# Performance work log

Measured on AMD Instinct MI355X. Metric: run time of the kernel, lower is better.

Reference implementation:

```python
import jax, jax.numpy as jnp
import numpy as np

N = 50000   # total nodes across batch of graphs
E = 600000  # edges (avg degree 12)
D = 128     # feature dim
L = 3       # GNN layers
B = 64      # number of graphs


def setup_inputs() -> dict:
    key = jax.random.key(0)
    ks = jax.random.split(key, 9)
    x = jax.random.normal(ks[0], (N, D), dtype=jnp.float32)
    edge_index = jax.random.randint(ks[1], (2, E), 0, N)
    batch = jnp.sort(jax.random.randint(ks[2], (N,), 0, B))
    # hard one-hot architecture gates (output of ST gumbel-softmax)
    z_agg = jax.nn.one_hot(jax.random.randint(ks[3], (L,), 0, 3), 3, dtype=jnp.float32)
    z_pool = jax.nn.one_hot(jax.random.randint(ks[4], (), 0, 3), 3, dtype=jnp.float32)
    scale = 1.0 / np.sqrt(D)
    W1 = jax.random.normal(ks[5], (L, D, D), dtype=jnp.float32) * scale
    b1 = jnp.zeros((L, D), dtype=jnp.float32)
    W2 = jax.random.normal(ks[6], (L, D, D), dtype=jnp.float32) * scale
    b2 = jnp.zeros((L, D), dtype=jnp.float32)
    return {"x": x, "edge_index": edge_index, "batch": batch,
            "z_agg": z_agg, "z_pool": z_pool,
            "W1": W1, "b1": b1, "W2": W2, "b2": b2}


def reference(x, edge_index, batch, z_agg, z_pool, W1, b1, W2, b2):
    src, dst = edge_index[0], edge_index[1]
    ones_e = jnp.ones((E,), dtype=x.dtype)
    deg = jax.ops.segment_sum(ones_e, dst, num_segments=N)          # [N]
    deg_c = jnp.maximum(deg, 1.0)[:, None]
    has_nb = (deg > 0)[:, None]

    for l in range(L):
        msg = x[src]                                                # [E, D] gather
        s = jax.ops.segment_sum(msg, dst, num_segments=N)           # sum aggr
        m = s / deg_c                                               # mean aggr
        mx = jax.ops.segment_max(msg, dst, num_segments=N)          # max aggr
        mx = jnp.where(has_nb, mx, 0.0)                             # PyG fills empty with 0
        agg = z_agg[l, 0] * s + z_agg[l, 1] * m + z_agg[l, 2] * mx
        # combine='sum' then FeedForwardNetwork: Linear->relu->Linear
        h = x + agg
        h = jnp.maximum(h @ W1[l] + b1[l], 0.0)
        h = h @ W2[l] + b2[l]
        # act='relu', layer_connect='skip_sum'
        x = x + jnp.maximum(h, 0.0)

    # global pooling mixture over batch vector
    ps = jax.ops.segment_sum(x, batch, num_segments=B)              # [B, D]
    cnt = jax.ops.segment_sum(jnp.ones((N,), x.dtype), batch, num_segments=B)
    pm = ps / jnp.maximum(cnt, 1.0)[:, None]
    pmx = jax.ops.segment_max(x, batch, num_segments=B)
    pmx = jnp.where((cnt > 0)[:, None], pmx, 0.0)
    return z_pool[0] * ps + z_pool[1] * pm + z_pool[2] * pmx
```

## Files before the change

kernel.cpp:

```cpp
#include <hip/hip_runtime.h>
#include <cfloat>

#define DD 128
#define NLAYERS 3
#define NPB 128
#define SCHUNK 1024

typedef short bf16x8 __attribute__((ext_vector_type(8)));
typedef float f32x4 __attribute__((ext_vector_type(4)));

__device__ __forceinline__ unsigned short f2b(float f) {
    unsigned u = __float_as_uint(f);
    u += 0x7fffu + ((u >> 16) & 1u);
    return (unsigned short)(u >> 16);
}
__device__ __forceinline__ float b2f(unsigned short b) {
    return __uint_as_float(((unsigned)b) << 16);
}

__device__ __forceinline__ unsigned enc_f(float f) {
    unsigned b = __float_as_uint(f);
    return (b & 0x80000000u) ? ~b : (b | 0x80000000u);
}
__device__ __forceinline__ float dec_f(unsigned u) {
    return __uint_as_float((u & 0x80000000u) ? (u & 0x7fffffffu) : ~u);
}


__global__ void convert_xb_kernel(const float* __restrict__ in,
                                  unsigned short* __restrict__ xb, int n4) {
    int i = blockIdx.x * blockDim.x + threadIdx.x;
    if (i >= n4) return;
    float4 v = ((const float4*)in)[i];
    ushort4 b;
    b.x = f2b(v.x); b.y = f2b(v.y); b.z = f2b(v.z); b.w = f2b(v.w);
    ((ushort4*)xb)[i] = b;
}

__global__ void convert_w_kernel(const float* __restrict__ W, unsigned short* __restrict__ Wb,
                                 int total) {
    int idx = blockIdx.x * blockDim.x + threadIdx.x;
    if (idx >= total) return;
    int lane = idx & 63;
    int rest = idx >> 6;
    int ks = rest & 3; rest >>= 2;
    int nt = rest & 7;
    int l  = rest >> 3;
    int n = nt * 16 + (lane & 15);
    int kbase = ks * 32 + (lane >> 4) * 8;
    const float* Wl = W + (size_t)l * DD * DD;
    unsigned short* dst = Wb + (size_t)l * DD * DD + ((size_t)(nt * 4 + ks) * 64 + lane) * 8;
#pragma unroll
    for (int j = 0; j < 8; ++j) dst[j] = f2b(Wl[(size_t)(kbase + j) * DD + n]);
}


__global__ void deg_kernel(const int* __restrict__ dst, int* __restrict__ deg, int nE) {
    int e = blockIdx.x * blockDim.x + threadIdx.x;
    if (e < nE) atomicAdd(&deg[dst[e]], 1);
}

__global__ __launch_bounds__(256) void scan_sum_kernel(const int* __restrict__ deg,
                                                       int* __restrict__ bsum, int nN) {
    int t = threadIdx.x;
    int base = blockIdx.x * SCHUNK + t * 4;
    int v = 0;
#pragma unroll
    for (int k = 0; k < 4; ++k) { int i = base + k; if (i < nN) v += deg[i]; }
    for (int off = 32; off; off >>= 1) v += __shfl_down(v, off, 64);
    __shared__ int wsum[4];
    if ((t & 63) == 0) wsum[t >> 6] = v;
    __syncthreads();
    if (t == 0) bsum[blockIdx.x] = wsum[0] + wsum[1] + wsum[2] + wsum[3];
}

__global__ __launch_bounds__(256) void scan_top_kernel(const int* __restrict__ bsum,
                                                       int* __restrict__ boff,
                                                       int* __restrict__ row_ptr,
                                                       int G, int nN) {
    __shared__ int sh[256];
    int t = threadIdx.x;
    int v = (t < G) ? bsum[t] : 0;
    sh[t] = v;
    __syncthreads();
    for (int off = 1; off < 256; off <<= 1) {
        int o = (t >= off) ? sh[t - off] : 0;
        __syncthreads();
        sh[t] += o;
        __syncthreads();
    }
    if (t < G) boff[t] = sh[t] - v;
    if (t == 255) row_ptr[nN] = sh[255];
}

__global__ __launch_bounds__(256) void scan_apply_kernel(const int* __restrict__ deg,
                                                         const int* __restrict__ boff,
                                                         int* __restrict__ row_ptr, int nN) {
    __shared__ int sh[256];
    int t = threadIdx.x;
    int base = blockIdx.x * SCHUNK + t * 4;
    int d0 = 0, d1 = 0, d2 = 0, d3 = 0;
    if (base + 0 < nN) d0 = deg[base + 0];
    if (base + 1 < nN) d1 = deg[base + 1];
    if (base + 2 < nN) d2 = deg[base + 2];
    if (base + 3 < nN) d3 = deg[base + 3];
    int tsum = d0 + d1 + d2 + d3;
    sh[t] = tsum;
    __syncthreads();
    for (int off = 1; off < 256; off <<= 1) {
        int o = (t >= off) ? sh[t - off] : 0;
        __syncthreads();
        sh[t] += o;
        __syncthreads();
    }
    int run = boff[blockIdx.x] + sh[t] - tsum;
    if (base + 0 < nN) row_ptr[base + 0] = run;           run += d0;
    if (base + 1 < nN) row_ptr[base + 1] = run;           run += d1;
    if (base + 2 < nN) row_ptr[base + 2] = run;           run += d2;
    if (base + 3 < nN) row_ptr[base + 3] = run;
}

__global__ void fill_kernel(const int* __restrict__ src, const int* __restrict__ dst,
                            const int* __restrict__ row_ptr, int* __restrict__ fill,
                            int* __restrict__ csr_src, int nE) {
    int e = blockIdx.x * blockDim.x + threadIdx.x;
    if (e >= nE) return;
    int d = dst[e];
    int pos = row_ptr[d] + atomicAdd(&fill[d], 1);
    csr_src[pos] = src[e];
}

__global__ __launch_bounds__(256) void agg_combine_kernel(const float* __restrict__ x,
                                                          const unsigned short* __restrict__ xb,
                                                          const int* __restrict__ csr_src,
                                                          const int* __restrict__ row_ptr,
                                                          const float* __restrict__ z_agg_l,
                                                          unsigned short* __restrict__ h0b,
                                                          int nN) {
    int t = threadIdx.x;
    int n = blockIdx.x * 8 + (t >> 5);
    if (n >= nN) return;
    int q = t & 31;
    int start = row_ptr[n], end = row_ptr[n + 1];
    float za0 = z_agg_l[0], za1 = z_agg_l[1], za2 = z_agg_l[2];

    const ushort4* tab = (const ushort4*)xb;
    float4 sum = make_float4(0.f, 0.f, 0.f, 0.f);
    float4 mx  = make_float4(-FLT_MAX, -FLT_MAX, -FLT_MAX, -FLT_MAX);
    int e = start;
    for (; e + 4 <= end; e += 4) {
        int s0 = csr_src[e + 0], s1 = csr_src[e + 1];
        int s2 = csr_src[e + 2], s3 = csr_src[e + 3];
        ushort4 v0 = tab[(size_t)s0 * 32 + q];
        ushort4 v1 = tab[(size_t)s1 * 32 + q];
        ushort4 v2 = tab[(size_t)s2 * 32 + q];
        ushort4 v3 = tab[(size_t)s3 * 32 + q];
#define ACC(vb) { float ax=b2f(vb.x),ay=b2f(vb.y),az=b2f(vb.z),aw=b2f(vb.w); \
                  sum.x+=ax;sum.y+=ay;sum.z+=az;sum.w+=aw; \
                  mx.x=fmaxf(mx.x,ax);mx.y=fmaxf(mx.y,ay); \
                  mx.z=fmaxf(mx.z,az);mx.w=fmaxf(mx.w,aw); }
        ACC(v0) ACC(v1) ACC(v2) ACC(v3)
    }
    for (; e < end; ++e) {
        int s0 = csr_src[e];
        ushort4 v0 = tab[(size_t)s0 * 32 + q];
        ACC(v0)
    }
#undef ACC
    int degn = end - start;
    float inv = 1.0f / fmaxf((float)degn, 1.0f);
    float c01 = za0 + za1 * inv;
    bool nb = (degn > 0);
    float4 xs = ((const float4*)(x + (size_t)n * DD))[q];
    ushort4 r;
    r.x = f2b(xs.x + c01 * sum.x + za2 * (nb ? mx.x : 0.f));
    r.y = f2b(xs.y + c01 * sum.y + za2 * (nb ? mx.y : 0.f));
    r.z = f2b(xs.z + c01 * sum.z + za2 * (nb ? mx.z : 0.f));
    r.w = f2b(xs.w + c01 * sum.w + za2 * (nb ? mx.w : 0.f));
    ((ushort4*)(h0b + (size_t)n * DD))[q] = r;
}

__global__ __launch_bounds__(256) void fused_ffn_kernel(
        const unsigned short* __restrict__ h0b,
        const unsigned short* __restrict__ Wb1, const float* __restrict__ b1,
        const unsigned short* __restrict__ Wb2, const float* __restrict__ b2,
        const float* __restrict__ x_in,
        float* __restrict__ x_out, unsigned short* __restrict__ xb_out, int M) {
    __shared__ char lds[64 * DD * 4];

    int t = threadIdx.x;
    int lane = t & 63;
    int w = t >> 6;
    int row0 = blockIdx.x * 64;
    int ar = row0 + w * 16 + (lane & 15);
    if (ar > M - 1) ar = M - 1;
    int g = lane >> 4;
    int colw = lane & 15;
    int rbl = w * 16 + g * 4;

    const unsigned short* Ap = h0b + (size_t)ar * DD + g * 8;
    bf16x8 a0 = *(const bf16x8*)(Ap);
    bf16x8 a1 = *(const bf16x8*)(Ap + 32);
    bf16x8 a2 = *(const bf16x8*)(Ap + 64);
    bf16x8 a3 = *(const bf16x8*)(Ap + 96);

    const bf16x8* Wv1 = (const bf16x8*)Wb1;
#pragma unroll
    for (int nt = 0; nt < 8; ++nt) {
        f32x4 acc = {0.f, 0.f, 0.f, 0.f};
        acc = __builtin_amdgcn_mfma_f32_16x16x32_bf16(a0, Wv1[(nt * 4 + 0) * 64 + lane], acc, 0, 0, 0);
        acc = __builtin_amdgcn_mfma_f32_16x16x32_bf16(a1, Wv1[(nt * 4 + 1) * 64 + lane], acc, 0, 0, 0);
        acc = __builtin_amdgcn_mfma_f32_16x16x32_bf16(a2, Wv1[(nt * 4 + 2) * 64 + lane], acc, 0, 0, 0);
        acc = __builtin_amdgcn_mfma_f32_16x16x32_bf16(a3, Wv1[(nt * 4 + 3) * 64 + lane], acc, 0, 0, 0);
        float bv = b1[nt * 16 + colw];
        int cb = (nt * 16 + colw) * 2;
#pragma unroll
        for (int i = 0; i < 4; ++i) {
            int r1 = rbl + i;
            *(unsigned short*)(lds + r1 * 256 + (cb ^ ((unsigned)(r1 & 7) << 4))) =
                f2b(fmaxf(acc[i] + bv, 0.f));
        }
    }

    int rAl = w * 16 + (lane & 15);
    unsigned swA = (unsigned)(rAl & 7) << 4;
    const char* hA = lds + rAl * 256;
    bf16x8 c0 = *(const bf16x8*)(hA + ((g * 16 +   0) ^ swA));
    bf16x8 c1 = *(const bf16x8*)(hA + ((g * 16 +  64) ^ swA));
    bf16x8 c2 = *(const bf16x8*)(hA + ((g * 16 + 128) ^ swA));
    bf16x8 c3 = *(const bf16x8*)(hA + ((g * 16 + 192) ^ swA));
    __syncthreads();

    const bf16x8* Wv2 = (const bf16x8*)Wb2;
#pragma unroll
    for (int nt = 0; nt < 8; ++nt) {
        f32x4 acc = {0.f, 0.f, 0.f, 0.f};
        acc = __builtin_amdgcn_mfma_f32_16x16x32_bf16(c0, Wv2[(nt * 4 + 0) * 64 + lane], acc, 0, 0, 0);
        acc = __builtin_amdgcn_mfma_f32_16x16x32_bf16(c1, Wv2[(nt * 4 + 1) * 64 + lane], acc, 0, 0, 0);
        acc = __builtin_amdgcn_mfma_f32_16x16x32_bf16(c2, Wv2[(nt * 4 + 2) * 64 + lane], acc, 0, 0, 0);
        acc = __builtin_amdgcn_mfma_f32_16x16x32_bf16(c3, Wv2[(nt * 4 + 3) * 64 + lane], acc, 0, 0, 0);
        float bv = b2[nt * 16 + colw];
        int cb = (nt * 16 + colw) * 4;
#pragma unroll
        for (int i = 0; i < 4; ++i) {
            int r1 = rbl + i;
            *(float*)(lds + r1 * 512 + (cb ^ ((unsigned)(r1 & 7) << 4))) =
                fmaxf(acc[i] + bv, 0.f);
        }
    }
    __syncthreads();

    int q = t & 31;
    int grp = t >> 5;
    for (int pass = 0; pass < 8; ++pass) {
        int rr = pass * 8 + grp;
        int n = row0 + rr;
        if (n < M) {
            float4 xv = ((const float4*)(x_in + (size_t)n * DD))[q];
            float4 vv = *(const float4*)(lds + rr * 512 + ((q * 16) ^ ((unsigned)(rr & 7) << 4)));
            float4 xo;
            xo.x = xv.x + vv.x; xo.y = xv.y + vv.y;
            xo.z = xv.z + vv.z; xo.w = xv.w + vv.w;
            ((float4*)(x_out + (size_t)n * DD))[q] = xo;
            ushort4 b;
            b.x = f2b(xo.x); b.y = f2b(xo.y); b.z = f2b(xo.z); b.w = f2b(xo.w);
            ((ushort4*)(xb_out + (size_t)n * DD))[q] = b;
        }
    }
}

__global__ __launch_bounds__(256) void pool_partial_kernel(const float* __restrict__ x,
                                                           const int* __restrict__ batch,
                                                           float* __restrict__ ps,
                                                           unsigned* __restrict__ pmx,
                                                           int* __restrict__ cnt, int nN) {
    int t = threadIdx.x;
    int q = t & 31;
    int p = t >> 5;
    int node0 = blockIdx.x * NPB;
    int nodeEnd = node0 + NPB; if (nodeEnd > nN) nodeEnd = nN;

    const float4* xv = (const float4*)x;
    float4 sum = make_float4(0.f, 0.f, 0.f, 0.f);
    float4 mx  = make_float4(-FLT_MAX, -FLT_MAX, -FLT_MAX, -FLT_MAX);
    int count = 0, g_cur = -1;

    for (int row = node0 + p; row < nodeEnd; row += 8) {
        int g = batch[row];
        if (g != g_cur) {
            if (g_cur >= 0) {
                atomicAdd(&ps[(size_t)g_cur * DD + q * 4 + 0], sum.x);
                atomicAdd(&ps[(size_t)g_cur * DD + q * 4 + 1], sum.y);
                atomicAdd(&ps[(size_t)g_cur * DD + q * 4 + 2], sum.z);
                atomicAdd(&ps[(size_t)g_cur * DD + q * 4 + 3], sum.w);
                atomicMax(&pmx[(size_t)g_cur * DD + q * 4 + 0], enc_f(mx.x));
                atomicMax(&pmx[(size_t)g_cur * DD + q * 4 + 1], enc_f(mx.y));
                atomicMax(&pmx[(size_t)g_cur * DD + q * 4 + 2], enc_f(mx.z));
                atomicMax(&pmx[(size_t)g_cur * DD + q * 4 + 3], enc_f(mx.w));
                if (q == 0) atomicAdd(&cnt[g_cur], count);
            }
            sum = make_float4(0.f, 0.f, 0.f, 0.f);
            mx  = make_float4(-FLT_MAX, -FLT_MAX, -FLT_MAX, -FLT_MAX);
            count = 0; g_cur = g;
        }
        float4 v = xv[(size_t)row * 32 + q];
        sum.x += v.x; sum.y += v.y; sum.z += v.z; sum.w += v.w;
        mx.x = fmaxf(mx.x, v.x); mx.y = fmaxf(mx.y, v.y);
        mx.z = fmaxf(mx.z, v.z); mx.w = fmaxf(mx.w, v.w);
        count++;
    }
    if (g_cur >= 0) {
        atomicAdd(&ps[(size_t)g_cur * DD + q * 4 + 0], sum.x);
        atomicAdd(&ps[(size_t)g_cur * DD + q * 4 + 1], sum.y);
        atomicAdd(&ps[(size_t)g_cur * DD + q * 4 + 2], sum.z);
        atomicAdd(&ps[(size_t)g_cur * DD + q * 4 + 3], sum.w);
        atomicMax(&pmx[(size_t)g_cur * DD + q * 4 + 0], enc_f(mx.x));
        atomicMax(&pmx[(size_t)g_cur * DD + q * 4 + 1], enc_f(mx.y));
        atomicMax(&pmx[(size_t)g_cur * DD + q * 4 + 2], enc_f(mx.z));
        atomicMax(&pmx[(size_t)g_cur * DD + q * 4 + 3], enc_f(mx.w));
        if (q == 0) atomicAdd(&cnt[g_cur], count);
    }
}

__global__ void pool_final_kernel(const float* __restrict__ ps,
                                  const unsigned* __restrict__ pmx,
                                  const int* __restrict__ cnt,
                                  const float* __restrict__ z_pool,
                                  float* __restrict__ out, int total) {
    int i = blockIdx.x * blockDim.x + threadIdx.x;
    if (i >= total) return;
    int g = i >> 7;
    float zp0 = z_pool[0], zp1 = z_pool[1], zp2 = z_pool[2];
    int c = cnt[g];
    float s = ps[i];
    float pm = s / fmaxf((float)c, 1.0f);
    float pv = (c > 0) ? dec_f(pmx[i]) : 0.0f;
    out[i] = zp0 * s + zp1 * pm + zp2 * pv;
}

extern "C" void kernel_launch(void* const* d_in, const int* in_sizes, int n_in,
                              void* d_out, int out_size, void* d_ws, size_t ws_size,
                              hipStream_t stream) {
    const float* x_in   = (const float*)d_in[0];
    const int*   eidx   = (const int*)d_in[1];
    const int*   batch  = (const int*)d_in[2];
    const float* z_agg  = (const float*)d_in[3];
    const float* z_pool = (const float*)d_in[4];
    const float* W1     = (const float*)d_in[5];
    const float* b1     = (const float*)d_in[6];
    const float* W2     = (const float*)d_in[7];
    const float* b2     = (const float*)d_in[8];

    int nN = in_sizes[0] / DD;
    int nE = in_sizes[1] / 2;
    int nB = out_size / DD;
    const int* src = eidx;
    const int* dst = eidx + nE;

    char* p = (char*)d_ws;
    size_t nd = (size_t)nN * DD * sizeof(float);
    float* xA           = (float*)p;           p += nd;
    float* xB           = (float*)p;           p += nd;
    unsigned short* xb0 = (unsigned short*)p;  p += nd / 2;
    unsigned short* xbA = (unsigned short*)p;  p += nd / 2;
    unsigned short* h0b = (unsigned short*)p;  p += nd / 2;
    unsigned short* Wb1 = (unsigned short*)p;  p += (size_t)NLAYERS * DD * DD * 2;
    unsigned short* Wb2 = (unsigned short*)p;  p += (size_t)NLAYERS * DD * DD * 2;
    int* row_ptr = (int*)p;  p += (size_t)(nN + 1) * 4;
    int* fill    = (int*)p;  p += (size_t)nN * 4;
    int* deg     = (int*)p;  p += (size_t)nN * 4;
    int* csr_src = (int*)p;  p += (size_t)nE * 4;
    float*    ps  = (float*)p;    p += (size_t)nB * DD * 4;
    unsigned* pmx = (unsigned*)p; p += (size_t)nB * DD * 4;
    int*      cnt = (int*)p;      p += (size_t)nB * 4;
    int*      bsum = (int*)p;     p += 256 * 4;
    int*      boff = (int*)p;

    int G = (nN + SCHUNK - 1) / SCHUNK;

    int n4 = nN * DD / 4;
    convert_xb_kernel<<<(n4 + 255) / 256, 256, 0, stream>>>(x_in, xb0, n4);
    int wgroups = NLAYERS * 8 * 4 * 64;
    convert_w_kernel<<<(wgroups + 255) / 256, 256, 0, stream>>>(W1, Wb1, wgroups);
    convert_w_kernel<<<(wgroups + 255) / 256, 256, 0, stream>>>(W2, Wb2, wgroups);

    hipMemsetAsync(deg, 0, (size_t)nN * sizeof(int), stream);
    hipMemsetAsync(fill, 0, (size_t)nN * sizeof(int), stream);
    deg_kernel<<<(nE + 255) / 256, 256, 0, stream>>>(dst, deg, nE);
    scan_sum_kernel<<<G, 256, 0, stream>>>(deg, bsum, nN);
    scan_top_kernel<<<1, 256, 0, stream>>>(bsum, boff, row_ptr, G, nN);
    scan_apply_kernel<<<G, 256, 0, stream>>>(deg, boff, row_ptr, nN);
    fill_kernel<<<(nE + 255) / 256, 256, 0, stream>>>(src, dst, row_ptr, fill, csr_src, nE);

    int agrid = (nN + 7) / 8;
    int fgrid = (nN + 63) / 64;
    agg_combine_kernel<<<agrid, 256, 0, stream>>>(x_in, xb0, csr_src, row_ptr,
                                                  z_agg + 0, h0b, nN);
    fused_ffn_kernel<<<fgrid, 256, 0, stream>>>(h0b, Wb1 + 0 * DD * DD, b1 + 0 * DD,
                                                Wb2 + 0 * DD * DD, b2 + 0 * DD,
                                                x_in, xA, xbA, nN);
    agg_combine_kernel<<<agrid, 256, 0, stream>>>(xA, xbA, csr_src, row_ptr,
                                                  z_agg + 3, h0b, nN);
    fused_ffn_kernel<<<fgrid, 256, 0, stream>>>(h0b, Wb1 + 1 * DD * DD, b1 + 1 * DD,
                                                Wb2 + 1 * DD * DD, b2 + 1 * DD,
                                                xA, xB, xb0, nN);
    agg_combine_kernel<<<agrid, 256, 0, stream>>>(xB, xb0, csr_src, row_ptr,
                                                  z_agg + 6, h0b, nN);
    fused_ffn_kernel<<<fgrid, 256, 0, stream>>>(h0b, Wb1 + 2 * DD * DD, b1 + 2 * DD,
                                                Wb2 + 2 * DD * DD, b2 + 2 * DD,
                                                xB, xA, xbA, nN);

    hipMemsetAsync(ps, 0, (size_t)nB * DD * sizeof(float), stream);
    hipMemsetAsync(pmx, 0, (size_t)nB * DD * sizeof(unsigned), stream);
    hipMemsetAsync(cnt, 0, (size_t)nB * sizeof(int), stream);
    pool_partial_kernel<<<(nN + NPB - 1) / NPB, 256, 0, stream>>>(xA, batch, ps, pmx, cnt, nN);
    pool_final_kernel<<<(nB * DD + 255) / 256, 256, 0, stream>>>(ps, pmx, cnt, z_pool,
                                                                 (float*)d_out, nB * DD);
}
```

Measured before the change: 282.8 us.

## Keep residual stream in bf16 only and fold memsets into conversion kernels

Drops the fp32 copies of the node features, so each layer reads and writes the residual only in bf16. Aggregation, the FFN epilogue and pooling all use the bf16 buffer, which cuts global memory traffic. It also folds the memsets into the convert kernel, merges the two weight conversions into one launch, and reuses the deg counter for CSR fill via atomicSub. The gather loop now fetches 8 neighbors per iteration with clamped indices to expose more parallel loads. The cost is bf16 rounding of the residual accumulated across layers, which adds numerical error.

After: 235.3 us. -16.8%, faster.

```diff
diff --git a/kernel.cpp b/kernel.cpp
--- a/kernel.cpp
+++ b/kernel.cpp
@@ -26,21 +26,32 @@
     return __uint_as_float((u & 0x80000000u) ? (u & 0x7fffffffu) : ~u);
 }
 
-
 __global__ void convert_xb_kernel(const float* __restrict__ in,
-                                  unsigned short* __restrict__ xb, int n4) {
+                                  unsigned short* __restrict__ xb,
+                                  int* __restrict__ deg,
+                                  float* __restrict__ ps, unsigned* __restrict__ pmx,
+                                  int* __restrict__ cnt,
+                                  int n4, int nN, int nBD, int nB) {
     int i = blockIdx.x * blockDim.x + threadIdx.x;
-    if (i >= n4) return;
-    float4 v = ((const float4*)in)[i];
-    ushort4 b;
-    b.x = f2b(v.x); b.y = f2b(v.y); b.z = f2b(v.z); b.w = f2b(v.w);
-    ((ushort4*)xb)[i] = b;
-}
-
-__global__ void convert_w_kernel(const float* __restrict__ W, unsigned short* __restrict__ Wb,
-                                 int total) {
+    if (i < n4) {
+        float4 v = ((const float4*)in)[i];
+        ushort4 b;
+        b.x = f2b(v.x); b.y = f2b(v.y); b.z = f2b(v.z); b.w = f2b(v.w);
+        ((ushort4*)xb)[i] = b;
+    }
+    if (i < nN) deg[i] = 0;
+    if (i < nBD) { ps[i] = 0.f; pmx[i] = 0u; }
+    if (i < nB) cnt[i] = 0;
+}
+
+__global__ void convert_w_kernel(const float* __restrict__ W1s, const float* __restrict__ W2s,
+                                 unsigned short* __restrict__ Wb1s,
+                                 unsigned short* __restrict__ Wb2s, int per) {
     int idx = blockIdx.x * blockDim.x + threadIdx.x;
-    if (idx >= total) return;
+    if (idx >= 2 * per) return;
+    const float* W = (idx < per) ? W1s : W2s;
+    unsigned short* Wb = (idx < per) ? Wb1s : Wb2s;
+    if (idx >= per) idx -= per;
     int lane = idx & 63;
     int rest = idx >> 6;
     int ks = rest & 3; rest >>= 2;
@@ -121,17 +132,16 @@
 }
 
 __global__ void fill_kernel(const int* __restrict__ src, const int* __restrict__ dst,
-                            const int* __restrict__ row_ptr, int* __restrict__ fill,
+                            const int* __restrict__ row_ptr, int* __restrict__ deg,
                             int* __restrict__ csr_src, int nE) {
     int e = blockIdx.x * blockDim.x + threadIdx.x;
     if (e >= nE) return;
     int d = dst[e];
-    int pos = row_ptr[d] + atomicAdd(&fill[d], 1);
+    int pos = row_ptr[d] + atomicSub(&deg[d], 1) - 1;
     csr_src[pos] = src[e];
 }
 
-__global__ __launch_bounds__(256) void agg_combine_kernel(const float* __restrict__ x,
-                                                          const unsigned short* __restrict__ xb,
+__global__ __launch_bounds__(256) void agg_combine_kernel(const unsigned short* __restrict__ xb,
                                                           const int* __restrict__ csr_src,
                                                           const int* __restrict__ row_ptr,
                                                           const float* __restrict__ z_agg_l,
@@ -147,36 +157,48 @@
     const ushort4* tab = (const ushort4*)xb;
     float4 sum = make_float4(0.f, 0.f, 0.f, 0.f);
     float4 mx  = make_float4(-FLT_MAX, -FLT_MAX, -FLT_MAX, -FLT_MAX);
-    int e = start;
-    for (; e + 4 <= end; e += 4) {
-        int s0 = csr_src[e + 0], s1 = csr_src[e + 1];
-        int s2 = csr_src[e + 2], s3 = csr_src[e + 3];
+    int last = end - 1;
+    for (int e = start; e < end; e += 8) {
+        int s0 = csr_src[e];
+        int s1 = csr_src[e + 1 <= last ? e + 1 : last];
+        int s2 = csr_src[e + 2 <= last ? e + 2 : last];
+        int s3 = csr_src[e + 3 <= last ? e + 3 : last];
+        int s4 = csr_src[e + 4 <= last ? e + 4 : last];
+        int s5 = csr_src[e + 5 <= last ? e + 5 : last];
+        int s6 = csr_src[e + 6 <= last ? e + 6 : last];
+        int s7 = csr_src[e + 7 <= last ? e + 7 : last];
         ushort4 v0 = tab[(size_t)s0 * 32 + q];
         ushort4 v1 = tab[(size_t)s1 * 32 + q];
         ushort4 v2 = tab[(size_t)s2 * 32 + q];
         ushort4 v3 = tab[(size_t)s3 * 32 + q];
-#define ACC(vb) { float ax=b2f(vb.x),ay=b2f(vb.y),az=b2f(vb.z),aw=b2f(vb.w); \
-                  sum.x+=ax;sum.y+=ay;sum.z+=az;sum.w+=aw; \
+        ushort4 v4 = tab[(size_t)s4 * 32 + q];
+        ushort4 v5 = tab[(size_t)s5 * 32 + q];
+        ushort4 v6 = tab[(size_t)s6 * 32 + q];
+        ushort4 v7 = tab[(size_t)s7 * 32 + q];
+#define ACCP(vb, ok) { float ax=b2f(vb.x),ay=b2f(vb.y),az=b2f(vb.z),aw=b2f(vb.w); \
                   mx.x=fmaxf(mx.x,ax);mx.y=fmaxf(mx.y,ay); \
-                  mx.z=fmaxf(mx.z,az);mx.w=fmaxf(mx.w,aw); }
-        ACC(v0) ACC(v1) ACC(v2) ACC(v3)
-    }
-    for (; e < end; ++e) {
-        int s0 = csr_src[e];
-        ushort4 v0 = tab[(size_t)s0 * 32 + q];
-        ACC(v0)
-    }
-#undef ACC
+                  mx.z=fmaxf(mx.z,az);mx.w=fmaxf(mx.w,aw); \
+                  if (ok) { sum.x+=ax;sum.y+=ay;sum.z+=az;sum.w+=aw; } }
+        ACCP(v0, true)
+        ACCP(v1, e + 1 < end)
+        ACCP(v2, e + 2 < end)
+        ACCP(v3, e + 3 < end)
+        ACCP(v4, e + 4 < end)
+        ACCP(v5, e + 5 < end)
+        ACCP(v6, e + 6 < end)
+        ACCP(v7, e + 7 < end)
+#undef ACCP
+    }
     int degn = end - start;
     float inv = 1.0f / fmaxf((float)degn, 1.0f);
     float c01 = za0 + za1 * inv;
     bool nb = (degn > 0);
-    float4 xs = ((const float4*)(x + (size_t)n * DD))[q];
+    ushort4 sb = tab[(size_t)n * 32 + q];
     ushort4 r;
-    r.x = f2b(xs.x + c01 * sum.x + za2 * (nb ? mx.x : 0.f));
-    r.y = f2b(xs.y + c01 * sum.y + za2 * (nb ? mx.y : 0.f));
-    r.z = f2b(xs.z + c01 * sum.z + za2 * (nb ? mx.z : 0.f));
-    r.w = f2b(xs.w + c01 * sum.w + za2 * (nb ? mx.w : 0.f));
+    r.x = f2b(b2f(sb.x) + c01 * sum.x + za2 * (nb ? mx.x : 0.f));
+    r.y = f2b(b2f(sb.y) + c01 * sum.y + za2 * (nb ? mx.y : 0.f));
+    r.z = f2b(b2f(sb.z) + c01 * sum.z + za2 * (nb ? mx.z : 0.f));
+    r.w = f2b(b2f(sb.w) + c01 * sum.w + za2 * (nb ? mx.w : 0.f));
     ((ushort4*)(h0b + (size_t)n * DD))[q] = r;
 }
 
@@ -184,8 +206,8 @@
         const unsigned short* __restrict__ h0b,
         const unsigned short* __restrict__ Wb1, const float* __restrict__ b1,
         const unsigned short* __restrict__ Wb2, const float* __restrict__ b2,
-        const float* __restrict__ x_in,
-        float* __restrict__ x_out, unsigned short* __restrict__ xb_out, int M) {
+        const unsigned short* __restrict__ xb_in,
+        unsigned short* __restrict__ xb_out, int M) {
     __shared__ char lds[64 * DD * 4];
 
     int t = threadIdx.x;
@@ -256,20 +278,19 @@
         int rr = pass * 8 + grp;
         int n = row0 + rr;
         if (n < M) {
-            float4 xv = ((const float4*)(x_in + (size_t)n * DD))[q];
+            ushort4 xv = ((const ushort4*)(xb_in + (size_t)n * DD))[q];
             float4 vv = *(const float4*)(lds + rr * 512 + ((q * 16) ^ ((unsigned)(rr & 7) << 4)));
-            float4 xo;
-            xo.x = xv.x + vv.x; xo.y = xv.y + vv.y;
-            xo.z = xv.z + vv.z; xo.w = xv.w + vv.w;
-            ((float4*)(x_out + (size_t)n * DD))[q] = xo;
             ushort4 b;
-            b.x = f2b(xo.x); b.y = f2b(xo.y); b.z = f2b(xo.z); b.w = f2b(xo.w);
+            b.x = f2b(b2f(xv.x) + vv.x);
+            b.y = f2b(b2f(xv.y) + vv.y);
+            b.z = f2b(b2f(xv.z) + vv.z);
+            b.w = f2b(b2f(xv.w) + vv.w);
             ((ushort4*)(xb_out + (size_t)n * DD))[q] = b;
         }
     }
 }
 
-__global__ __launch_bounds__(256) void pool_partial_kernel(const float* __restrict__ x,
+__global__ __launch_bounds__(256) void pool_partial_kernel(const unsigned short* __restrict__ xb,
                                                            const int* __restrict__ batch,
                                                            float* __restrict__ ps,
                                                            unsigned* __restrict__ pmx,
@@ -280,7 +301,7 @@
     int node0 = blockIdx.x * NPB;
     int nodeEnd = node0 + NPB; if (nodeEnd > nN) nodeEnd = nN;
 
-    const float4* xv = (const float4*)x;
+    const ushort4* xv = (const ushort4*)xb;
     float4 sum = make_float4(0.f, 0.f, 0.f, 0.f);
     float4 mx  = make_float4(-FLT_MAX, -FLT_MAX, -FLT_MAX, -FLT_MAX);
     int count = 0, g_cur = -1;
@@ -303,10 +324,11 @@
             mx  = make_float4(-FLT_MAX, -FLT_MAX, -FLT_MAX, -FLT_MAX);
             count = 0; g_cur = g;
         }
-        float4 v = xv[(size_t)row * 32 + q];
-        sum.x += v.x; sum.y += v.y; sum.z += v.z; sum.w += v.w;
-        mx.x = fmaxf(mx.x, v.x); mx.y = fmaxf(mx.y, v.y);
-        mx.z = fmaxf(mx.z, v.z); mx.w = fmaxf(mx.w, v.w);
+        ushort4 vb = xv[(size_t)row * 32 + q];
+        float vx = b2f(vb.x), vy = b2f(vb.y), vz = b2f(vb.z), vw = b2f(vb.w);
+        sum.x += vx; sum.y += vy; sum.z += vz; sum.w += vw;
+        mx.x = fmaxf(mx.x, vx); mx.y = fmaxf(mx.y, vy);
+        mx.z = fmaxf(mx.z, vz); mx.w = fmaxf(mx.w, vw);
         count++;
     }
     if (g_cur >= 0) {
@@ -359,15 +381,12 @@
 
     char* p = (char*)d_ws;
     size_t nd = (size_t)nN * DD * sizeof(float);
-    float* xA           = (float*)p;           p += nd;
-    float* xB           = (float*)p;           p += nd;
     unsigned short* xb0 = (unsigned short*)p;  p += nd / 2;
     unsigned short* xbA = (unsigned short*)p;  p += nd / 2;
     unsigned short* h0b = (unsigned short*)p;  p += nd / 2;
     unsigned short* Wb1 = (unsigned short*)p;  p += (size_t)NLAYERS * DD * DD * 2;
     unsigned short* Wb2 = (unsigned short*)p;  p += (size_t)NLAYERS * DD * DD * 2;
     int* row_ptr = (int*)p;  p += (size_t)(nN + 1) * 4;
-    int* fill    = (int*)p;  p += (size_t)nN * 4;
     int* deg     = (int*)p;  p += (size_t)nN * 4;
     int* csr_src = (int*)p;  p += (size_t)nE * 4;
     float*    ps  = (float*)p;    p += (size_t)nB * DD * 4;
@@ -379,41 +398,33 @@
     int G = (nN + SCHUNK - 1) / SCHUNK;
 
     int n4 = nN * DD / 4;
-    convert_xb_kernel<<<(n4 + 255) / 256, 256, 0, stream>>>(x_in, xb0, n4);
-    int wgroups = NLAYERS * 8 * 4 * 64;
-    convert_w_kernel<<<(wgroups + 255) / 256, 256, 0, stream>>>(W1, Wb1, wgroups);
-    convert_w_kernel<<<(wgroups + 255) / 256, 256, 0, stream>>>(W2, Wb2, wgroups);
-
-    hipMemsetAsync(deg, 0, (size_t)nN * sizeof(int), stream);
-    hipMemsetAsync(fill, 0, (size_t)nN * sizeof(int), stream);
+    convert_xb_kernel<<<(n4 + 255) / 256, 256, 0, stream>>>(x_in, xb0, deg, ps, pmx, cnt,
+                                                            n4, nN, nB * DD, nB);
+    int per = NLAYERS * 8 * 4 * 64;
+    convert_w_kernel<<<(2 * per + 255) / 256, 256, 0, stream>>>(W1, W2, Wb1, Wb2, per);
+
     deg_kernel<<<(nE + 255) / 256, 256, 0, stream>>>(dst, deg, nE);
     scan_sum_kernel<<<G, 256, 0, stream>>>(deg, bsum, nN);
     scan_top_kernel<<<1, 256, 0, stream>>>(bsum, boff, row_ptr, G, nN);
     scan_apply_kernel<<<G, 256, 0, stream>>>(deg, boff, row_ptr, nN);
-    fill_kernel<<<(nE + 255) / 256, 256, 0, stream>>>(src, dst, row_ptr, fill, csr_src, nE);
+    fill_kernel<<<(nE + 255) / 256, 256, 0, stream>>>(src, dst, row_ptr, deg, csr_src, nE);
 
     int agrid = (nN + 7) / 8;
     int fgrid = (nN + 63) / 64;
-    agg_combine_kernel<<<agrid, 256, 0, stream>>>(x_in, xb0, csr_src, row_ptr,
-                                                  z_agg + 0, h0b, nN);
+    agg_combine_kernel<<<agrid, 256, 0, stream>>>(xb0, csr_src, row_ptr, z_agg + 0, h0b, nN);
     fused_ffn_kernel<<<fgrid, 256, 0, stream>>>(h0b, Wb1 + 0 * DD * DD, b1 + 0 * DD,
                                                 Wb2 + 0 * DD * DD, b2 + 0 * DD,
-                                                x_in, xA, xbA, nN);
-    agg_combine_kernel<<<agrid, 256, 0, stream>>>(xA, xbA, csr_src, row_ptr,
-                                                  z_agg + 3, h0b, nN);
+                                                xb0, xbA, nN);
+    agg_combine_kernel<<<agrid, 256, 0, stream>>>(xbA, csr_src, row_ptr, z_agg + 3, h0b, nN);
     fused_ffn_kernel<<<fgrid, 256, 0, stream>>>(h0b, Wb1 + 1 * DD * DD, b1 + 1 * DD,
                                                 Wb2 + 1 * DD * DD, b2 + 1 * DD,
-                                                xA, xB, xb0, nN);
-    agg_combine_kernel<<<agrid, 256, 0, stream>>>(xB, xb0, csr_src, row_ptr,
-                                                  z_agg + 6, h0b, nN);
+                                                xbA, xb0, nN);
+    agg_combine_kernel<<<agrid, 256, 0, stream>>>(xb0, csr_src, row_ptr, z_agg + 6, h0b, nN);
     fused_ffn_kernel<<<fgrid, 256, 0, stream>>>(h0b, Wb1 + 2 * DD * DD, b1 + 2 * DD,
                                                 Wb2 + 2 * DD * DD, b2 + 2 * DD,
-                                                xB, xA, xbA, nN);
-
-    hipMemsetAsync(ps, 0, (size_t)nB * DD * sizeof(float), stream);
-    hipMemsetAsync(pmx, 0, (size_t)nB * DD * sizeof(unsigned), stream);
-    hipMemsetAsync(cnt, 0, (size_t)nB * sizeof(int), stream);
-    pool_partial_kernel<<<(nN + NPB - 1) / NPB, 256, 0, stream>>>(xA, batch, ps, pmx, cnt, nN);
+                                                xb0, xbA, nN);
+
+    pool_partial_kernel<<<(nN + NPB - 1) / NPB, 256, 0, stream>>>(xbA, batch, ps, pmx, cnt, nN);
     pool_final_kernel<<<(nB * DD + 255) / 256, 256, 0, stream>>>(ps, pmx, cnt, z_pool,
                                                                  (float*)d_out, nB * DD);
 }
```
